# Kernel tuning notes

Hardware: AMD Instinct MI355X
Metric: run time of the kernel (lower is better)

## Reference

```python
import jax, jax.numpy as jnp
import numpy as np


def _gru_dir(x, kernel, rec_kernel, bias):
    """Keras GRU (reset_after=True). x: [B,T,D] -> [B,T,U]."""
    B, T, D = x.shape
    U = rec_kernel.shape[0]
    # Precompute input projections for all timesteps: [B,T,3U]
    xw = jnp.einsum('btd,dk->btk', x, kernel) + bias[0]
    h0 = jnp.zeros((B, U), dtype=x.dtype)

    def step(h, xw_t):
        rec = h @ rec_kernel + bias[1]            # [B,3U]
        xz, xr, xh = jnp.split(xw_t, 3, axis=-1)
        rz, rr, rh = jnp.split(rec, 3, axis=-1)
        z = jax.nn.sigmoid(xz + rz)
        r = jax.nn.sigmoid(xr + rr)
        hh = jnp.tanh(xh + r * rh)
        h_new = z * h + (1.0 - z) * hh
        return h_new, h_new

    _, hs = jax.lax.scan(step, h0, jnp.swapaxes(xw, 0, 1))  # hs: [T,B,U]
    return jnp.swapaxes(hs, 0, 1)


def setup_inputs() -> dict:
    key = jax.random.key(0)
    ks = jax.random.split(key, 7)
    B, T, D, U = 64, 1024, 256, 256
    s_in = 1.0 / np.sqrt(D)
    s_rec = 1.0 / np.sqrt(U)
    return {
        'x': jax.random.normal(ks[0], (B, T, D), jnp.float32),
        'kernel_f': jax.random.normal(ks[1], (D, 3 * U), jnp.float32) * s_in,
        'rec_kernel_f': jax.random.normal(ks[2], (U, 3 * U), jnp.float32) * s_rec,
        'bias_f': jnp.zeros((2, 3 * U), jnp.float32),
        'kernel_b': jax.random.normal(ks[3], (D, 3 * U), jnp.float32) * s_in,
        'rec_kernel_b': jax.random.normal(ks[4], (U, 3 * U), jnp.float32) * s_rec,
        'bias_b': jnp.zeros((2, 3 * U), jnp.float32),
    }


def reference(x, kernel_f, rec_kernel_f, bias_f, kernel_b, rec_kernel_b, bias_b):
    # Forward direction
    out_f = _gru_dir(x, kernel_f, rec_kernel_f, bias_f)
    # Backward direction: reverse time, run GRU, reverse output back
    xb = x[:, ::-1, :]
    out_b = _gru_dir(xb, kernel_b, rec_kernel_b, bias_b)[:, ::-1, :]
    # Bidirectional merge_mode='concat'
    return jnp.concatenate([out_f, out_b], axis=-1)  # [B,T,2U]
```

## Files before the change

kernel.cpp:

```cpp
#include <hip/hip_runtime.h>
#include <hip/hip_fp16.h>
#include <hip/hip_bf16.h>

typedef __attribute__((ext_vector_type(8))) short bf16x8;
typedef __attribute__((ext_vector_type(4))) float f32x4;
typedef __attribute__((ext_vector_type(2))) __fp16 f16x2;

__device__ __forceinline__ short f2bf(float f) {
    unsigned u = __builtin_bit_cast(unsigned, f);
    unsigned r = (u + 0x7FFFu + ((u >> 16) & 1u)) >> 16;
    return (short)r;
}
__device__ __forceinline__ float fast_rcp(float x) {
    return __builtin_amdgcn_rcpf(x);
}
__device__ __forceinline__ float fast_exp(float x) {
    return __builtin_amdgcn_exp2f(x * 1.4426950408889634f);
}

__global__ __launch_bounds__(256) void prep_kernel(
    const float* __restrict__ kf, const float* __restrict__ kb,
    const float* __restrict__ rf, const float* __restrict__ rb,
    short* __restrict__ kT, short* __restrict__ rTf, short* __restrict__ rTb)
{
    int idx = blockIdx.x * 256 + threadIdx.x;
    int n = idx >> 8;
    int k = idx & 255;
    const float* src = (n < 768) ? kf : kb;
    int nn = (n < 768) ? n : (n - 768);
    kT[idx] = f2bf(src[k * 768 + nn]);
    if (n < 768) {
        rTf[idx] = f2bf(rf[k * 768 + n]);
        rTb[idx] = f2bf(rb[k * 768 + n]);
    }
}

__global__ __launch_bounds__(256) void proj_kernel(
    const float* __restrict__ x, const short* __restrict__ kT,
    const float* __restrict__ bias_f, const float* __restrict__ bias_b,
    char* __restrict__ xwp_f, char* __restrict__ xwp_b)
{
    __shared__ short lA[64][264];
    __shared__ short lB[128][264];

    const int tid = threadIdx.x;
    const int bt   = blockIdx.x;
    const int tbase16 = (bt >> 4) * 16;
    const int bg   = (bt & 15) >> 2;
    const int hi_t = bt & 3;
    const int n0 = blockIdx.y * 128;

#pragma unroll
    for (int rep = 0; rep < 16; ++rep) {
        int lin = rep * 256 + tid;
        int r = lin >> 6;
        int c4 = lin & 63;
        int bb = bg * 16 + hi_t * 4 + (r & 3);
        int tt = tbase16 + (r >> 2);
        float4 v = *(const float4*)(x + ((size_t)bb * 1024 + tt) * 256 + c4 * 4);
        short4 s;
        s.x = f2bf(v.x); s.y = f2bf(v.y); s.z = f2bf(v.z); s.w = f2bf(v.w);
        *(short4*)&lA[r][c4 * 4] = s;
    }
#pragma unroll
    for (int rep = 0; rep < 16; ++rep) {
        int lin = rep * 256 + tid;
        int r = lin >> 5;
        int c8 = lin & 31;
        uint4 v = *(const uint4*)(kT + (size_t)(n0 + r) * 256 + c8 * 8);
        *(uint4*)&lB[r][c8 * 8] = v;
    }
    __syncthreads();

    const int w = tid >> 6, l = tid & 63;
    const int l15 = l & 15, hi = l >> 4;

    bf16x8 a[8];
#pragma unroll
    for (int kt = 0; kt < 8; ++kt)
        a[kt] = *(const bf16x8*)&lA[w * 16 + l15][kt * 32 + hi * 8];

    const int t_row   = tbase16 + w * 4 + hi;
    const int lane_t  = hi_t * 16 + l15;

#pragma unroll
    for (int j = 0; j < 8; ++j) {
        f32x4 acc = {0.f, 0.f, 0.f, 0.f};
#pragma unroll
        for (int kt = 0; kt < 8; ++kt) {
            bf16x8 b = *(const bf16x8*)&lB[j * 16 + l15][kt * 32 + hi * 8];
            acc = __builtin_amdgcn_mfma_f32_16x16x32_bf16(a[kt], b, acc, 0, 0, 0);
        }
        int ng   = n0 + j * 16;
        int dirb = ng >= 768;
        int nn0  = ng - (dirb ? 768 : 0);
        int g    = nn0 >> 8;
        int wtj  = (nn0 & 255) >> 4;
        const float* bias = dirb ? bias_b : bias_f;
        char* basep = dirb ? xwp_b : xwp_f;
        int nn = nn0 + l15;
        float badd = bias[nn] + ((nn < 512) ? bias[768 + nn] : 0.f);

        f16x2 lo2 = __builtin_amdgcn_cvt_pkrtz(acc[0] + badd, acc[1] + badd);
        f16x2 hi2 = __builtin_amdgcn_cvt_pkrtz(acc[2] + badd, acc[3] + badd);
        uint2 pk;
        pk.x = __builtin_bit_cast(unsigned, lo2);
        pk.y = __builtin_bit_cast(unsigned, hi2);

        if (g < 2) {
            *(uint2*)(basep + ((size_t)bg << 24) + ((size_t)t_row << 14)
                      + (wtj << 10) + (lane_t << 4) + (g * 8)) = pk;
        } else {
            *(uint2*)(basep + 67108864u + ((size_t)bg << 23)
                      + ((size_t)t_row << 13) + (wtj << 9) + (lane_t << 3)) = pk;
        }
    }
}

#define GRU_STEP(PR, PW)                                                     \
  {                                                                          \
    uint4  xv16 = *(const uint4*)xp16;  xp16 += step16;                      \
    uint2  xv8  = *(const uint2*)xp8;   xp8  += step8;                       \
    unsigned bbase = 0;                                                      \
    asm volatile("" : "+v"(bbase));    \
    f32x4 az = {0.f,0.f,0.f,0.f}, ar = {0.f,0.f,0.f,0.f},                    \
          ah = {0.f,0.f,0.f,0.f};                                           \
    _Pragma("unroll") for (int kt = 0; kt < 8; ++kt) {                       \
      bf16x8 aq = *(const bf16x8*)((const char*)hfrag + (PR)*8192            \
                                   + kt * 1024 + l * 16);                    \
      bf16x8 bh;                                                             \
      if (kt < 5) bh = Bh[kt];                                               \
      else bh = *(const bf16x8*)((const char*)bfrag + bbase                  \
                                 + (kt - 5) * 16384 + w * 1024 + l * 16);    \
      az = __builtin_amdgcn_mfma_f32_16x16x32_bf16(aq, Bz[kt], az, 0,0,0);   \
      ar = __builtin_amdgcn_mfma_f32_16x16x32_bf16(aq, Br[kt], ar, 0,0,0);   \
      ah = __builtin_amdgcn_mfma_f32_16x16x32_bf16(aq, bh, ah, 0,0,0);       \
    }                                                                        \
    const __half* hx  = (const __half*)&xv16;                                \
    const __half* hx8 = (const __half*)&xv8;                                 \
    float hn[4];                                                             \
    _Pragma("unroll") for (int i = 0; i < 4; ++i) {                          \
      float zi  = fast_rcp(1.f + fast_exp(-(__half2float(hx[i]) + az[i])));  \
      float rri = fast_rcp(1.f + fast_exp(-(__half2float(hx[4+i]) + ar[i])));\
      float pre = __half2float(hx8[i]) + rri * (ah[i] + b1h);                \
      float sg  = fast_rcp(1.f + fast_exp(-2.f * pre));                      \
      float hh  = 2.f * sg - 1.f;                                            \
      float h2  = hh + zi * (hold[i] - hh);                                  \
      hold[i] = h2;  hn[i] = h2;                                             \
      opbase[i * 524288] = h2;                                               \
    }                                                                        \
    unsigned pk0, pk1;                                                       \
    asm("v_cvt_pk_bf16_f32 %0, %1, %2" : "=v"(pk0) : "v"(hn[0]), "v"(hn[1]));\
    asm("v_cvt_pk_bf16_f32 %0, %1, %2" : "=v"(pk1) : "v"(hn[2]), "v"(hn[3]));\
    {                                                                        \
      char* hb = (char*)hfrag + (PW)*8192 + wb;                              \
      *(short*)(hb)      = (short)(pk0 & 0xffff);                            \
      *(short*)(hb + 16) = (short)(pk0 >> 16);                               \
      *(short*)(hb + 32) = (short)(pk1 & 0xffff);                            \
      *(short*)(hb + 48) = (short)(pk1 >> 16);                               \
    }                                                                        \
    opbase += ostep;                                                         \
    asm volatile("s_waitcnt lgkmcnt(0)\n\ts_barrier" ::: "memory");          \
  }

__global__ __launch_bounds__(1024) void gru_kernel(
    const char* __restrict__ xwp_f, const char* __restrict__ xwp_b,
    const short* __restrict__ recT_f, const short* __restrict__ recT_b,
    const float* __restrict__ bias_f, const float* __restrict__ bias_b,
    float* __restrict__ out)
{
    __shared__ short hfrag[2][8][64][8];
    __shared__ short bfrag[3][16][64][8];

    const int tid = threadIdx.x;
    const int w = tid >> 6, l = tid & 63;
    const int l15 = l & 15, hi = l >> 4;
    const int dir = blockIdx.x >> 2;
    const int bg  = blockIdx.x & 3;
    const int b0  = bg * 16;

    const char*  xwp  = dir ? xwp_b  : xwp_f;
    const short* recT = dir ? recT_b : recT_f;
    const float* bias = dir ? bias_b : bias_f;

    const int cg = w * 16 + l15;
    const float b1h = bias[768 + 512 + cg];

    ((int4*)hfrag)[tid] = make_int4(0, 0, 0, 0);

    const char* recTc = (const char*)recT;
    unsigned offz = (((unsigned)(cg)       * 256u) + hi * 8u) * 2u;
    unsigned offr = (((unsigned)(256 + cg) * 256u) + hi * 8u) * 2u;
    unsigned offh = (((unsigned)(512 + cg) * 256u) + hi * 8u) * 2u;
    bf16x8 Bz[8], Br[8], Bh[5];
#pragma unroll
    for (int kt = 0; kt < 8; ++kt) {
        Bz[kt] = *(const bf16x8*)(recTc + offz + kt * 64);
        Br[kt] = *(const bf16x8*)(recTc + offr + kt * 64);
    }
#pragma unroll
    for (int kt = 0; kt < 5; ++kt)
        Bh[kt] = *(const bf16x8*)(recTc + offh + kt * 64);
#pragma unroll
    for (int kt = 5; kt < 8; ++kt) {
        bf16x8 tmp = *(const bf16x8*)(recTc + offh + kt * 64);
        *(bf16x8*)((char*)bfrag + (kt - 5) * 16384 + w * 1024 + l * 16) = tmp;
    }

    const int t0 = dir ? 1023 : 0;
    const long step16 = dir ? -16384 : 16384;
    const long step8  = dir ? -8192  : 8192;
    const char* xp16 = xwp + ((size_t)bg << 24) + ((size_t)t0 << 14)
                       + (w << 10) + (l << 4);
    const char* xp8  = xwp + 67108864u + ((size_t)bg << 23) + ((size_t)t0 << 13)
                       + (w << 9) + (l << 3);

    const long ostep = dir ? -512 : 512;
    float* opbase = out + (size_t)(b0 + hi * 4) * 524288 + (size_t)t0 * 512
                    + (size_t)dir * 256 + cg;

    const unsigned wb = (unsigned)(cg >> 5) * 1024u
                      + ((((unsigned)cg >> 3) & 3u) * 16u) * 16u
                      + (unsigned)(hi * 4) * 16u + ((unsigned)(l15 & 7)) * 2u;

    f32x4 hold = {0.f, 0.f, 0.f, 0.f};
    __syncthreads();

    for (int su = 0; su < 512; ++su) {
        GRU_STEP(0, 1)
        GRU_STEP(1, 0)
    }
}

extern "C" void kernel_launch(void* const* d_in, const int* in_sizes, int n_in,
                              void* d_out, int out_size, void* d_ws, size_t ws_size,
                              hipStream_t stream) {
    const float* x   = (const float*)d_in[0];
    const float* kf  = (const float*)d_in[1];
    const float* rf  = (const float*)d_in[2];
    const float* bf_ = (const float*)d_in[3];
    const float* kb  = (const float*)d_in[4];
    const float* rb  = (const float*)d_in[5];
    const float* bb_ = (const float*)d_in[6];

    char* ws = (char*)d_ws;
    char* xwp_f = ws;
    char* xwp_b = ws + 100663296;
    short* rTf  = (short*)(ws + 201326592);
    short* rTb  = (short*)(ws + 201719808);
    short* kT   = (short*)(ws + 202113024);
    float* out  = (float*)d_out;

    hipLaunchKernelGGL(prep_kernel, dim3(1536), dim3(256), 0, stream,
                       kf, kb, rf, rb, kT, rTf, rTb);
    hipLaunchKernelGGL(proj_kernel, dim3(1024, 12), dim3(256), 0, stream,
                       x, kT, bf_, bb_, xwp_f, xwp_b);
    hipLaunchKernelGGL(gru_kernel, dim3(8), dim3(1024), 0, stream,
                       xwp_f, xwp_b, rTf, rTb, bf_, bb_, out);
}
```

Baseline: 1.779 ms.

## Split GRU recurrence into 16 blocks of 8 batch rows with two column tiles per wave

```diff
diff --git a/kernel.cpp b/kernel.cpp
--- a/kernel.cpp
+++ b/kernel.cpp
@@ -5,6 +5,9 @@
 typedef __attribute__((ext_vector_type(8))) short bf16x8;
 typedef __attribute__((ext_vector_type(4))) float f32x4;
 typedef __attribute__((ext_vector_type(2))) __fp16 f16x2;
+
+#define L2E  1.4426950408889634f
+#define L2E2 2.8853901817779268f
 
 __device__ __forceinline__ short f2bf(float f) {
     unsigned u = __builtin_bit_cast(unsigned, f);
@@ -14,8 +17,13 @@
 __device__ __forceinline__ float fast_rcp(float x) {
     return __builtin_amdgcn_rcpf(x);
 }
-__device__ __forceinline__ float fast_exp(float x) {
-    return __builtin_amdgcn_exp2f(x * 1.4426950408889634f);
+__device__ __forceinline__ float exp2n(float x) {
+    return __builtin_amdgcn_exp2f(-x);
+}
+__device__ __forceinline__ float pl32_lo(float a, float b) {
+    auto r = __builtin_amdgcn_permlane32_swap(
+        __builtin_bit_cast(int, a), __builtin_bit_cast(int, b), false, false);
+    return __builtin_bit_cast(float, r[0]);
 }
 
 __global__ __launch_bounds__(256) void prep_kernel(
@@ -28,10 +36,12 @@
     int k = idx & 255;
     const float* src = (n < 768) ? kf : kb;
     int nn = (n < 768) ? n : (n - 768);
-    kT[idx] = f2bf(src[k * 768 + nn]);
+    float sc = (nn < 512) ? L2E : L2E2;
+    kT[idx] = f2bf(src[k * 768 + nn] * sc);
     if (n < 768) {
-        rTf[idx] = f2bf(rf[k * 768 + n]);
-        rTb[idx] = f2bf(rb[k * 768 + n]);
+        float sc2 = (n < 512) ? L2E : L2E2;
+        rTf[idx] = f2bf(rf[k * 768 + n] * sc2);
+        rTb[idx] = f2bf(rb[k * 768 + n] * sc2);
     }
 }
 
@@ -44,10 +54,10 @@
     __shared__ short lB[128][264];
 
     const int tid = threadIdx.x;
-    const int bt   = blockIdx.x;
+    const int bt = blockIdx.x;
     const int tbase16 = (bt >> 4) * 16;
-    const int bg   = (bt & 15) >> 2;
-    const int hi_t = bt & 3;
+    const int bgrp   = (bt & 15) >> 1;
+    const int hi_row = bt & 1;
     const int n0 = blockIdx.y * 128;
 
 #pragma unroll
@@ -55,7 +65,7 @@
         int lin = rep * 256 + tid;
         int r = lin >> 6;
         int c4 = lin & 63;
-        int bb = bg * 16 + hi_t * 4 + (r & 3);
+        int bb = bgrp * 8 + hi_row * 4 + (r & 3);
         int tt = tbase16 + (r >> 2);
         float4 v = *(const float4*)(x + ((size_t)bb * 1024 + tt) * 256 + c4 * 4);
         short4 s;
@@ -80,8 +90,7 @@
     for (int kt = 0; kt < 8; ++kt)
         a[kt] = *(const bf16x8*)&lA[w * 16 + l15][kt * 32 + hi * 8];
 
-    const int t_row   = tbase16 + w * 4 + hi;
-    const int lane_t  = hi_t * 16 + l15;
+    const int t_row = tbase16 + w * 4 + hi;
 
 #pragma unroll
     for (int j = 0; j < 8; ++j) {
@@ -95,11 +104,15 @@
         int dirb = ng >= 768;
         int nn0  = ng - (dirb ? 768 : 0);
         int g    = nn0 >> 8;
-        int wtj  = (nn0 & 255) >> 4;
+        int cg2  = nn0 & 255;
+        int wtj  = cg2 >> 5;
+        int tb   = (cg2 >> 4) & 1;
+        int lane_t = tb * 32 + hi_row * 16 + l15;
         const float* bias = dirb ? bias_b : bias_f;
         char* basep = dirb ? xwp_b : xwp_f;
         int nn = nn0 + l15;
-        float badd = bias[nn] + ((nn < 512) ? bias[768 + nn] : 0.f);
+        float sc = (nn < 512) ? L2E : L2E2;
+        float badd = (bias[nn] + ((nn < 512) ? bias[768 + nn] : 0.f)) * sc;
 
         f16x2 lo2 = __builtin_amdgcn_cvt_pkrtz(acc[0] + badd, acc[1] + badd);
         f16x2 hi2 = __builtin_amdgcn_cvt_pkrtz(acc[2] + badd, acc[3] + badd);
@@ -108,43 +121,61 @@
         pk.y = __builtin_bit_cast(unsigned, hi2);
 
         if (g < 2) {
-            *(uint2*)(basep + ((size_t)bg << 24) + ((size_t)t_row << 14)
+            *(uint2*)(basep + ((size_t)bgrp << 23) + ((size_t)t_row << 13)
                       + (wtj << 10) + (lane_t << 4) + (g * 8)) = pk;
         } else {
-            *(uint2*)(basep + 67108864u + ((size_t)bg << 23)
-                      + ((size_t)t_row << 13) + (wtj << 9) + (lane_t << 3)) = pk;
+            *(uint2*)(basep + 67108864u + ((size_t)bgrp << 22)
+                      + ((size_t)t_row << 12) + (wtj << 9) + (lane_t << 3)) = pk;
         }
     }
 }
 
-#define GRU_STEP(PR, PW)                                                     \
+#define MFMA_BF16(A, B, C) __builtin_amdgcn_mfma_f32_16x16x32_bf16(A, B, C, 0, 0, 0)
+
+#define GRU_STEP(PR, PW, XC16, XC8, XN16, XN8)                               \
   {                                                                          \
-    uint4  xv16 = *(const uint4*)xp16;  xp16 += step16;                      \
-    uint2  xv8  = *(const uint2*)xp8;   xp8  += step8;                       \
-    unsigned bbase = 0;                                                      \
-    asm volatile("" : "+v"(bbase));    \
-    f32x4 az = {0.f,0.f,0.f,0.f}, ar = {0.f,0.f,0.f,0.f},                    \
-          ah = {0.f,0.f,0.f,0.f};                                           \
+    XN16 = *(const uint4*)xp16;  xp16 += step16;                             \
+    XN8  = *(const uint2*)xp8;   xp8  += step8;                              \
+    unsigned bb = 0;                                                         \
+    asm volatile("" : "+v"(bb));       \
+    f32x4 a0z={0.f,0.f,0.f,0.f}, a0r={0.f,0.f,0.f,0.f};                      \
+    f32x4 a0h={b1h0,b1h0,b1h0,b1h0};                                         \
+    f32x4 a1z={0.f,0.f,0.f,0.f}, a1r={0.f,0.f,0.f,0.f};                      \
+    f32x4 a1h={b1h1,b1h1,b1h1,b1h1};                                         \
     _Pragma("unroll") for (int kt = 0; kt < 8; ++kt) {                       \
       bf16x8 aq = *(const bf16x8*)((const char*)hfrag + (PR)*8192            \
                                    + kt * 1024 + l * 16);                    \
-      bf16x8 bh;                                                             \
-      if (kt < 5) bh = Bh[kt];                                               \
-      else bh = *(const bf16x8*)((const char*)bfrag + bbase                  \
-                                 + (kt - 5) * 16384 + w * 1024 + l * 16);    \
-      az = __builtin_amdgcn_mfma_f32_16x16x32_bf16(aq, Bz[kt], az, 0,0,0);   \
-      ar = __builtin_amdgcn_mfma_f32_16x16x32_bf16(aq, Br[kt], ar, 0,0,0);   \
-      ah = __builtin_amdgcn_mfma_f32_16x16x32_bf16(aq, bh, ah, 0,0,0);       \
+      bf16x8 bh0v, bh1v;                                                     \
+      if (kt < 5) { bh0v = Bh0[kt]; bh1v = Bh1[kt]; }                        \
+      else {                                                                 \
+        bh0v = *(const bf16x8*)(bfragc + bb + (kt - 5) * 8192                \
+                                + w * 1024 + l * 16);                        \
+        bh1v = *(const bf16x8*)(bfragc + bb + 24576 + (kt - 5) * 8192        \
+                                + w * 1024 + l * 16);                        \
+      }                                                                      \
+      a0z = MFMA_BF16(aq, Bz0[kt], a0z);                                     \
+      a0r = MFMA_BF16(aq, Br0[kt], a0r);                                     \
+      a0h = MFMA_BF16(aq, bh0v,    a0h);                                     \
+      a1z = MFMA_BF16(aq, Bz1[kt], a1z);                                     \
+      a1r = MFMA_BF16(aq, Br1[kt], a1r);                                     \
+      a1h = MFMA_BF16(aq, bh1v,    a1h);                                     \
     }                                                                        \
-    const __half* hx  = (const __half*)&xv16;                                \
-    const __half* hx8 = (const __half*)&xv8;                                 \
+    _Pragma("unroll") for (int i = 0; i < 4; ++i) {                          \
+      a0z[i] = pl32_lo(a0z[i], a1z[i]);                                      \
+      a0r[i] = pl32_lo(a0r[i], a1r[i]);                                      \
+      a0h[i] = pl32_lo(a0h[i], a1h[i]);                                      \
+    }                                                                        \
+    const __half* hx  = (const __half*)&XC16;                                \
+    const __half* hx8 = (const __half*)&XC8;                                 \
     float hn[4];                                                             \
     _Pragma("unroll") for (int i = 0; i < 4; ++i) {                          \
-      float zi  = fast_rcp(1.f + fast_exp(-(__half2float(hx[i]) + az[i])));  \
-      float rri = fast_rcp(1.f + fast_exp(-(__half2float(hx[4+i]) + ar[i])));\
-      float pre = __half2float(hx8[i]) + rri * (ah[i] + b1h);                \
-      float sg  = fast_rcp(1.f + fast_exp(-2.f * pre));                      \
-      float hh  = 2.f * sg - 1.f;                                            \
+      float az  = __half2float(hx[i])     + a0z[i];                          \
+      float ar  = __half2float(hx[4 + i]) + a0r[i];                          \
+      float zi  = fast_rcp(1.f + exp2n(az));                                 \
+      float rri = fast_rcp(1.f + exp2n(ar));                                 \
+      float pre = __fmaf_rn(rri, a0h[i], __half2float(hx8[i]));              \
+      float q   = fast_rcp(1.f + exp2n(pre));                                \
+      float hh  = 2.f * q - 1.f;                                             \
       float h2  = hh + zi * (hold[i] - hh);                                  \
       hold[i] = h2;  hn[i] = h2;                                             \
       opbase[i * 524288] = h2;                                               \
@@ -163,72 +194,89 @@
     asm volatile("s_waitcnt lgkmcnt(0)\n\ts_barrier" ::: "memory");          \
   }
 
-__global__ __launch_bounds__(1024) void gru_kernel(
+__global__ __launch_bounds__(512) void gru_kernel(
     const char* __restrict__ xwp_f, const char* __restrict__ xwp_b,
     const short* __restrict__ recT_f, const short* __restrict__ recT_b,
     const float* __restrict__ bias_f, const float* __restrict__ bias_b,
     float* __restrict__ out)
 {
     __shared__ short hfrag[2][8][64][8];
-    __shared__ short bfrag[3][16][64][8];
+    __shared__ short bfrag[2][3][8][64][8];
 
     const int tid = threadIdx.x;
     const int w = tid >> 6, l = tid & 63;
     const int l15 = l & 15, hi = l >> 4;
-    const int dir = blockIdx.x >> 2;
-    const int bg  = blockIdx.x & 3;
-    const int b0  = bg * 16;
+    const int dir  = blockIdx.x >> 3;
+    const int bgrp = blockIdx.x & 7;
 
     const char*  xwp  = dir ? xwp_b  : xwp_f;
     const short* recT = dir ? recT_b : recT_f;
     const float* bias = dir ? bias_b : bias_f;
 
-    const int cg = w * 16 + l15;
-    const float b1h = bias[768 + 512 + cg];
-
-    ((int4*)hfrag)[tid] = make_int4(0, 0, 0, 0);
+    const int cg0 = w * 32 + l15;
+    const float b1h0 = bias[1280 + cg0] * L2E2;
+    const float b1h1 = bias[1280 + cg0 + 16] * L2E2;
+
+    const int tile    = hi >> 1;
+    const int cme     = w * 32 + tile * 16 + l15;
+    const int rowbase = (hi & 1) * 4;
+
+    ((int4*)hfrag)[tid]       = make_int4(0, 0, 0, 0);
+    ((int4*)hfrag)[tid + 512] = make_int4(0, 0, 0, 0);
 
     const char* recTc = (const char*)recT;
-    unsigned offz = (((unsigned)(cg)       * 256u) + hi * 8u) * 2u;
-    unsigned offr = (((unsigned)(256 + cg) * 256u) + hi * 8u) * 2u;
-    unsigned offh = (((unsigned)(512 + cg) * 256u) + hi * 8u) * 2u;
-    bf16x8 Bz[8], Br[8], Bh[5];
+    const char* bfragc = (const char*)bfrag;
+    unsigned offz = (((unsigned)(cg0)       * 256u) + hi * 8u) * 2u;
+    unsigned offr = (((unsigned)(256 + cg0) * 256u) + hi * 8u) * 2u;
+    unsigned offh = (((unsigned)(512 + cg0) * 256u) + hi * 8u) * 2u;
+    bf16x8 Bz0[8], Br0[8], Bz1[8], Br1[8], Bh0[5], Bh1[5];
 #pragma unroll
     for (int kt = 0; kt < 8; ++kt) {
-        Bz[kt] = *(const bf16x8*)(recTc + offz + kt * 64);
-        Br[kt] = *(const bf16x8*)(recTc + offr + kt * 64);
-    }
-#pragma unroll
-    for (int kt = 0; kt < 5; ++kt)
-        Bh[kt] = *(const bf16x8*)(recTc + offh + kt * 64);
+        Bz0[kt] = *(const bf16x8*)(recTc + offz + kt * 64);
+        Br0[kt] = *(const bf16x8*)(recTc + offr + kt * 64);
+        Bz1[kt] = *(const bf16x8*)(recTc + offz + 8192 + kt * 64);
+        Br1[kt] = *(const bf16x8*)(recTc + offr + 8192 + kt * 64);
+    }
+#pragma unroll
+    for (int kt = 0; kt < 5; ++kt) {
+        Bh0[kt] = *(const bf16x8*)(recTc + offh + kt * 64);
+        Bh1[kt] = *(const bf16x8*)(recTc + offh + 8192 + kt * 64);
+    }
 #pragma unroll
     for (int kt = 5; kt < 8; ++kt) {
-        bf16x8 tmp = *(const bf16x8*)(recTc + offh + kt * 64);
-        *(bf16x8*)((char*)bfrag + (kt - 5) * 16384 + w * 1024 + l * 16) = tmp;
+        bf16x8 t0v = *(const bf16x8*)(recTc + offh + kt * 64);
+        bf16x8 t1v = *(const bf16x8*)(recTc + offh + 8192 + kt * 64);
+        *(bf16x8*)((char*)bfrag + (kt - 5) * 8192 + w * 1024 + l * 16) = t0v;
+        *(bf16x8*)((char*)bfrag + 24576 + (kt - 5) * 8192 + w * 1024 + l * 16) = t1v;
     }
 
     const int t0 = dir ? 1023 : 0;
-    const long step16 = dir ? -16384 : 16384;
-    const long step8  = dir ? -8192  : 8192;
-    const char* xp16 = xwp + ((size_t)bg << 24) + ((size_t)t0 << 14)
+    const long step16 = dir ? -8192 : 8192;
+    const long step8  = dir ? -4096 : 4096;
+    const char* xp16 = xwp + ((size_t)bgrp << 23) + ((size_t)t0 << 13)
                        + (w << 10) + (l << 4);
-    const char* xp8  = xwp + 67108864u + ((size_t)bg << 23) + ((size_t)t0 << 13)
+    const char* xp8  = xwp + 67108864u + ((size_t)bgrp << 22) + ((size_t)t0 << 12)
                        + (w << 9) + (l << 3);
 
     const long ostep = dir ? -512 : 512;
-    float* opbase = out + (size_t)(b0 + hi * 4) * 524288 + (size_t)t0 * 512
-                    + (size_t)dir * 256 + cg;
-
-    const unsigned wb = (unsigned)(cg >> 5) * 1024u
-                      + ((((unsigned)cg >> 3) & 3u) * 16u) * 16u
-                      + (unsigned)(hi * 4) * 16u + ((unsigned)(l15 & 7)) * 2u;
+    float* opbase = out + (size_t)(bgrp * 8 + rowbase) * 524288
+                    + (size_t)t0 * 512 + (size_t)dir * 256 + cme;
+
+    const unsigned wb = (unsigned)(cme >> 5) * 1024u
+                      + (unsigned)((cme >> 3) & 3) * 256u
+                      + (unsigned)rowbase * 16u + (unsigned)(cme & 7) * 2u;
+
+    uint4 xA16, xB16;
+    uint2 xA8,  xB8;
+    xA16 = *(const uint4*)xp16;  xp16 += step16;
+    xA8  = *(const uint2*)xp8;   xp8  += step8;
 
     f32x4 hold = {0.f, 0.f, 0.f, 0.f};
     __syncthreads();
 
     for (int su = 0; su < 512; ++su) {
-        GRU_STEP(0, 1)
-        GRU_STEP(1, 0)
+        GRU_STEP(0, 1, xA16, xA8, xB16, xB8)
+        GRU_STEP(1, 0, xB16, xB8, xA16, xA8)
     }
 }
 
@@ -255,6 +303,6 @@
                        kf, kb, rf, rb, kT, rTf, rTb);
     hipLaunchKernelGGL(proj_kernel, dim3(1024, 12), dim3(256), 0, stream,
                        x, kT, bf_, bb_, xwp_f, xwp_b);
-    hipLaunchKernelGGL(gru_kernel, dim3(8), dim3(1024), 0, stream,
+    hipLaunchKernelGGL(gru_kernel, dim3(16), dim3(512), 0, stream,
                        xwp_f, xwp_b, rTf, rTb, bf_, bb_, out);
 }
```

Result: no change. 1.807 ms (+1.6%).
